# Kernel tuning notes

Hardware: AMD Instinct MI355X
Metric: run time of the kernel (lower is better)

The kernel has to match this reference:

```python
import jax, jax.numpy as jnp
import numpy as np

B, S, D = 2, 2048, 4096
NH, NKV, HD = 32, 8, 128
NREP = NH // NKV
ROPE_THETA = 10000.0


def setup_inputs() -> dict:
    key = jax.random.key(0)
    k1, k2, k3, k4, k5 = jax.random.split(key, 5)
    x = jax.random.normal(k1, (B, S, D), jnp.float32)
    wq = jax.random.normal(k2, (NH * HD, D), jnp.float32) * 0.02
    wk = jax.random.normal(k3, (NKV * HD, D), jnp.float32) * 0.02
    wv = jax.random.normal(k4, (NKV * HD, D), jnp.float32) * 0.02
    wo = jax.random.normal(k5, (D, NH * HD), jnp.float32) * 0.02
    inv_freq = 1.0 / (ROPE_THETA ** (np.arange(0, HD, 2, dtype=np.float64) / HD))
    ang = np.outer(np.arange(S, dtype=np.float64), inv_freq)  # [S, HD/2]
    return {
        'x': x, 'start_pos': 0,
        'freqs_cos': jnp.asarray(np.cos(ang), jnp.float32),
        'freqs_sin': jnp.asarray(np.sin(ang), jnp.float32),
        'wq': wq, 'wk': wk, 'wv': wv, 'wo': wo,
    }


def _apply_rope(x, cos, sin):
    # x: [B, S, H, HD]; cos/sin: [S, HD/2]. Matches torch view_as_complex on
    # interleaved (even, odd) feature pairs: (xr + i*xi) * (cos + i*sin).
    xr = x[..., 0::2]
    xi = x[..., 1::2]
    c = cos[None, :, None, :]
    s = sin[None, :, None, :]
    out_r = xr * c - xi * s
    out_i = xr * s + xi * c
    return jnp.stack([out_r, out_i], axis=-1).reshape(x.shape)


def reference(x, start_pos, freqs_cos, freqs_sin, wq, wk, wv, wo):
    b, s, _ = x.shape
    xq = (x @ wq.T).reshape(b, s, NH, HD)
    xk = (x @ wk.T).reshape(b, s, NKV, HD)
    xv = (x @ wv.T).reshape(b, s, NKV, HD)
    # Source applies RoPE to K and V (not Q) -- reproduced faithfully.
    xk = _apply_rope(xk, freqs_cos, freqs_sin)
    xv = _apply_rope(xv, freqs_cos, freqs_sin)
    # start_pos == 0 prefill: cache slice [:, :start_pos+s] == freshly written xk/xv.
    # repeat_kv: head h_out = h_kv * NREP + rep  ==  jnp.repeat along head axis.
    keys = jnp.repeat(xk, NREP, axis=2)    # [B, S, NH, HD]
    values = jnp.repeat(xv, NREP, axis=2)  # [B, S, NH, HD]
    scale = 1.0 / jnp.sqrt(jnp.asarray(HD, x.dtype))
    scores = jnp.einsum('bqhd,bkhd->bhqk', xq, keys) * scale  # [B, NH, S, S]
    probs = jax.nn.softmax(scores, axis=-1)  # NOTE: no causal mask in source
    out = jnp.einsum('bhqk,bkhd->bqhd', probs, values).reshape(b, s, NH * HD)
    return out @ wo.T
```

## Files before the change

### kernel.cpp

```cpp
#include <hip/hip_runtime.h>


typedef short bf16x8 __attribute__((ext_vector_type(8)));
typedef float f32x4 __attribute__((ext_vector_type(4)));

__device__ __forceinline__ void load16(const void* g, void* l) {
  __builtin_amdgcn_global_load_lds(
      (const __attribute__((address_space(1))) void*)g,
      (__attribute__((address_space(3))) void*)l, 16, 0, 0);
}

__device__ __forceinline__ f32x4 mfma16(bf16x8 a, bf16x8 b, f32x4 c) {
  return __builtin_amdgcn_mfma_f32_16x16x32_bf16(a, b, c, 0, 0, 0);
}

__device__ __forceinline__ unsigned short f2b(float f) {
  union { float f; unsigned int u; } v; v.f = f;
  unsigned int u = v.u;
  return (unsigned short)((u + 0x7fffu + ((u >> 16) & 1u)) >> 16);
}
__device__ __forceinline__ float b2f(unsigned short u) {
  union { unsigned int u; float f; } v; v.u = ((unsigned int)u) << 16;
  return v.f;
}

#define QSCALE (0.08838834764831845f * 1.4426950408889634f)

__global__ __launch_bounds__(256) void cvt_f32_bf16(
    const float* __restrict__ in, unsigned short* __restrict__ out, int n4) {
  int idx = blockIdx.x * 256 + threadIdx.x;
  int stride = gridDim.x * 256;
  for (int i = idx; i < n4; i += stride) {
    float4 v = reinterpret_cast<const float4*>(in)[i];
    ushort4 o;
    o.x = f2b(v.x); o.y = f2b(v.y); o.z = f2b(v.z); o.w = f2b(v.w);
    reinterpret_cast<ushort4*>(out)[i] = o;
  }
}

template <typename OutT, bool SCALEQ>
__global__ __launch_bounds__(512, 2) void gemm256(
    const unsigned short* __restrict__ A, const unsigned short* __restrict__ Bw,
    OutT* __restrict__ C, int M, int N, int K) {
  extern __shared__ char smem[];
  const int tid = threadIdx.x;
  const int lane = tid & 63;
  const int w = tid >> 6;
  const int lr = lane & 15, lg = lane >> 4;
  const int wr = w >> 2, wc = w & 3;

  const int nbn = N >> 8;
  const int bid = blockIdx.x, nwg = gridDim.x;
  const int swz = (bid & 7) * (nwg >> 3) + (bid >> 3);
  const int bm = swz / nbn, bn = swz % nbn;

  const unsigned short* Ag = A + (size_t)bm * 256 * K;
  const unsigned short* Bg = Bw + (size_t)bn * 256 * K;

  int srow[4], skhw[4], sdst[4];
#pragma unroll
  for (int j = 0; j < 4; ++j) {
    const int c = tid + j * 512;
    srow[j] = c >> 3;
    skhw[j] = ((c & 7) ^ ((c >> 3) & 7)) << 3;
    sdst[j] = ((tid & ~63) << 4) + j * 8192;
  }

  f32x4 acc[8][4];
#pragma unroll
  for (int m = 0; m < 8; ++m)
#pragma unroll
    for (int n = 0; n < 4; ++n) acc[m][n] = (f32x4){0.f, 0.f, 0.f, 0.f};

#define STAGEA4(tt)                                                           \
  {                                                                           \
    char* d = smem + (((tt)&1) * 65536);                                      \
    _Pragma("unroll") for (int j = 0; j < 4; ++j)                             \
        load16(Ag + (size_t)srow[j] * K + ((tt) << 6) + skhw[j], d + sdst[j]);\
  }
#define STAGEB4(tt)                                                           \
  {                                                                           \
    char* d = smem + (((tt)&1) * 65536) + 32768;                              \
    _Pragma("unroll") for (int j = 0; j < 4; ++j)                             \
        load16(Bg + (size_t)srow[j] * K + ((tt) << 6) + skhw[j], d + sdst[j]);\
  }

  STAGEB4(0);
  STAGEA4(0);

  const int NT = K >> 6;
  const int rx = (lr & 7) << 4;
  const int aRow0 = (wr * 128 + lr) * 128;
  const int bRow0 = (wc * 64 + lr) * 128;
  const int col0 = (lg * 16) ^ rx;
  const int col1 = (64 + lg * 16) ^ rx;

  bf16x8 aR[4][2], bR[4][2];

  for (int t = 0; t < NT; ++t) {
    const char* bufA = smem + (t & 1) * 65536;
    const char* bufB = bufA + 32768;
    const bool more = (t + 1) < NT;

    asm volatile("s_waitcnt vmcnt(0)" ::: "memory");
    __builtin_amdgcn_s_barrier();

#pragma unroll
    for (int mf = 0; mf < 4; ++mf) {
      aR[mf][0] = *(const bf16x8*)(bufA + aRow0 + mf * 2048 + col0);
      aR[mf][1] = *(const bf16x8*)(bufA + aRow0 + mf * 2048 + col1);
    }
#pragma unroll
    for (int nf = 0; nf < 2; ++nf) {
      bR[nf][0] = *(const bf16x8*)(bufB + bRow0 + nf * 2048 + col0);
      bR[nf][1] = *(const bf16x8*)(bufB + bRow0 + nf * 2048 + col1);
    }
    if (more) STAGEB4(t + 1);
    asm volatile("s_waitcnt lgkmcnt(8)" ::: "memory");
    __builtin_amdgcn_s_barrier();
    asm volatile("s_waitcnt lgkmcnt(0)" ::: "memory");
    __builtin_amdgcn_sched_barrier(0);
    __builtin_amdgcn_s_setprio(1);
#pragma unroll
    for (int mf = 0; mf < 4; ++mf)
#pragma unroll
      for (int nf = 0; nf < 2; ++nf) {
        acc[mf][nf] = mfma16(aR[mf][0], bR[nf][0], acc[mf][nf]);
        acc[mf][nf] = mfma16(aR[mf][1], bR[nf][1], acc[mf][nf]);
      }
    __builtin_amdgcn_s_setprio(0);
    __builtin_amdgcn_s_barrier();

#pragma unroll
    for (int nf = 2; nf < 4; ++nf) {
      bR[nf][0] = *(const bf16x8*)(bufB + bRow0 + nf * 2048 + col0);
      bR[nf][1] = *(const bf16x8*)(bufB + bRow0 + nf * 2048 + col1);
    }
    if (more) STAGEA4(t + 1);
    __builtin_amdgcn_s_barrier();
    asm volatile("s_waitcnt lgkmcnt(0)" ::: "memory");
    __builtin_amdgcn_sched_barrier(0);
    __builtin_amdgcn_s_setprio(1);
#pragma unroll
    for (int mf = 0; mf < 4; ++mf)
#pragma unroll
      for (int nf = 2; nf < 4; ++nf) {
        acc[mf][nf] = mfma16(aR[mf][0], bR[nf][0], acc[mf][nf]);
        acc[mf][nf] = mfma16(aR[mf][1], bR[nf][1], acc[mf][nf]);
      }
    __builtin_amdgcn_s_setprio(0);
    __builtin_amdgcn_s_barrier();

#pragma unroll
    for (int mf = 0; mf < 4; ++mf) {
      aR[mf][0] = *(const bf16x8*)(bufA + aRow0 + (4 + mf) * 2048 + col0);
      aR[mf][1] = *(const bf16x8*)(bufA + aRow0 + (4 + mf) * 2048 + col1);
    }
    __builtin_amdgcn_s_barrier();
    asm volatile("s_waitcnt lgkmcnt(0)" ::: "memory");
    __builtin_amdgcn_sched_barrier(0);
    __builtin_amdgcn_s_setprio(1);
#pragma unroll
    for (int mf = 0; mf < 4; ++mf)
#pragma unroll
      for (int nf = 0; nf < 2; ++nf) {
        acc[4 + mf][nf] = mfma16(aR[mf][0], bR[nf][0], acc[4 + mf][nf]);
        acc[4 + mf][nf] = mfma16(aR[mf][1], bR[nf][1], acc[4 + mf][nf]);
      }
    __builtin_amdgcn_s_setprio(0);
    __builtin_amdgcn_s_barrier();

    __builtin_amdgcn_s_setprio(1);
#pragma unroll
    for (int mf = 0; mf < 4; ++mf)
#pragma unroll
      for (int nf = 2; nf < 4; ++nf) {
        acc[4 + mf][nf] = mfma16(aR[mf][0], bR[nf][0], acc[4 + mf][nf]);
        acc[4 + mf][nf] = mfma16(aR[mf][1], bR[nf][1], acc[4 + mf][nf]);
      }
    __builtin_amdgcn_s_setprio(0);
  }
#undef STAGEA4
#undef STAGEB4

#pragma unroll
  for (int mf = 0; mf < 8; ++mf)
#pragma unroll
    for (int nf = 0; nf < 4; ++nf)
#pragma unroll
      for (int r = 0; r < 4; ++r) {
        int rowc = bm * 256 + wr * 128 + mf * 16 + lg * 4 + r;
        int colc = bn * 256 + wc * 64 + nf * 16 + lr;
        float v = acc[mf][nf][r];
        if constexpr (SCALEQ) v *= QSCALE;
        if constexpr (sizeof(OutT) == 2)
          C[(size_t)rowc * N + colc] = (OutT)f2b(v);
        else
          C[(size_t)rowc * N + colc] = v;
      }
}

template <typename OutT>
__global__ __launch_bounds__(256) void gemm_bt(
    const unsigned short* __restrict__ A, const unsigned short* __restrict__ Bw,
    OutT* __restrict__ C, int M, int N, int K) {
  alignas(16) __shared__ unsigned short As[4][128][8];
  alignas(16) __shared__ unsigned short Bs[4][128][8];
  const int t = threadIdx.x;
  const int lane = t & 63, w = t >> 6;
  const int lr = lane & 15, lg = lane >> 4;
  const int wr = w >> 1, wc = w & 1;

  const int nbn = N >> 7;
  const int nwg = gridDim.x;
  const int bid = blockIdx.x;
  const int swz = (bid & 7) * (nwg >> 3) + (bid >> 3);
  const int bm = swz / nbn, bn = swz % nbn;

  f32x4 acc[4][4];
#pragma unroll
  for (int m = 0; m < 4; ++m)
#pragma unroll
    for (int n = 0; n < 4; ++n) acc[m][n] = (f32x4){0.f, 0.f, 0.f, 0.f};

  const int c0 = t, c1 = 256 + t;
  const int kc0 = c0 >> 7, row0 = c0 & 127;
  const int kc1 = c1 >> 7, row1 = c1 & 127;
  const unsigned short* Ab = A + (size_t)(bm * 128) * K;
  const unsigned short* Bb = Bw + (size_t)(bn * 128) * K;
  char* AsB = (char*)&As[0][0][0];
  char* BsB = (char*)&Bs[0][0][0];
  const int ub0 = (t & 192) * 16;
  const int ub1 = (256 + (t & 192)) * 16;

  for (int k0 = 0; k0 < K; k0 += 32) {
    load16(Ab + (size_t)row0 * K + k0 + kc0 * 8, AsB + ub0);
    load16(Ab + (size_t)row1 * K + k0 + kc1 * 8, AsB + ub1);
    load16(Bb + (size_t)row0 * K + k0 + kc0 * 8, BsB + ub0);
    load16(Bb + (size_t)row1 * K + k0 + kc1 * 8, BsB + ub1);
    __syncthreads();
    bf16x8 af[4], bfr[4];
#pragma unroll
    for (int i = 0; i < 4; ++i)
      af[i] = *(const bf16x8*)&As[lg][wr * 64 + i * 16 + lr][0];
#pragma unroll
    for (int i = 0; i < 4; ++i)
      bfr[i] = *(const bf16x8*)&Bs[lg][wc * 64 + i * 16 + lr][0];
#pragma unroll
    for (int m = 0; m < 4; ++m)
#pragma unroll
      for (int n = 0; n < 4; ++n)
        acc[m][n] = mfma16(af[m], bfr[n], acc[m][n]);
    __syncthreads();
  }

#pragma unroll
  for (int m = 0; m < 4; ++m)
#pragma unroll
    for (int n = 0; n < 4; ++n)
#pragma unroll
      for (int r = 0; r < 4; ++r) {
        int rowc = bm * 128 + wr * 64 + m * 16 + lg * 4 + r;
        int colc = bn * 128 + wc * 64 + n * 16 + lr;
        float v = acc[m][n][r];
        if constexpr (sizeof(OutT) == 2)
          C[(size_t)rowc * N + colc] = (OutT)f2b(v);
        else
          C[(size_t)rowc * N + colc] = v;
      }
}

__global__ __launch_bounds__(256) void rope_kv(
    const unsigned short* __restrict__ XKV,
    const float* __restrict__ fc, const float* __restrict__ fs,
    unsigned short* __restrict__ Kr, unsigned short* __restrict__ Vt) {
  __shared__ unsigned short Vl[128][66];
  const int t = threadIdx.x;
  const int bid = blockIdx.x;
  const int stile = bid & 31, bkv = bid >> 5;
  const int b = bkv >> 3, kvh = bkv & 7;
  const int s0 = stile * 64;
  const int l = t & 63;
  const int jrow = t >> 6;

  for (int j = 0; j < 16; ++j) {
    int s = s0 + j * 4 + jrow;
    ushort2 v = *(const ushort2*)(XKV + (size_t)(b * 2048 + s) * 2048 + kvh * 128 + 2 * l);
    float c = fc[s * 64 + l], sn = fs[s * 64 + l];
    float xr = b2f(v.x), xi = b2f(v.y);
    ushort2 o;
    o.x = f2b(xr * c - xi * sn);
    o.y = f2b(xr * sn + xi * c);
    *(ushort2*)(Kr + ((size_t)bkv * 2048 + s) * 128 + 2 * l) = o;
  }
  for (int j = 0; j < 16; ++j) {
    int ss = j * 4 + jrow;
    int s = s0 + ss;
    ushort2 v = *(const ushort2*)(XKV + (size_t)(b * 2048 + s) * 2048 + 1024 + kvh * 128 + 2 * l);
    float c = fc[s * 64 + l], sn = fs[s * 64 + l];
    float xr = b2f(v.x), xi = b2f(v.y);
    Vl[2 * l][ss] = f2b(xr * c - xi * sn);
    Vl[2 * l + 1][ss] = f2b(xr * sn + xi * c);
  }
  __syncthreads();
  const int d = t >> 1, half = t & 1;
  unsigned short* vdst = Vt + ((size_t)bkv * 128 + d) * 2048 + s0 + half * 32;
#pragma unroll
  for (int e = 0; e < 32; e += 4) {
    ushort4 pk;
    pk.x = Vl[d][half * 32 + e];
    pk.y = Vl[d][half * 32 + e + 1];
    pk.z = Vl[d][half * 32 + e + 2];
    pk.w = Vl[d][half * 32 + e + 3];
    *(ushort4*)(vdst + e) = pk;
  }
}

__global__ __launch_bounds__(256, 2) void attn_fwd(
    const unsigned short* __restrict__ XQ, const unsigned short* __restrict__ Kr,
    const unsigned short* __restrict__ Vt, unsigned short* __restrict__ AO) {
  extern __shared__ char smem[];
  char* Ksm = smem;
  char* Vsm = smem + 32768;
  unsigned short* Ps = (unsigned short*)(smem + 65536);
  const int t = threadIdx.x;
  const int lane = t & 63, w = t >> 6;
  const int lr = lane & 15, lg = lane >> 4;

  const int bid = blockIdx.x;
  const int nwg = gridDim.x;
  const int swz = (bid & 7) * (nwg >> 3) + (bid >> 3);
  const int qt = swz & 15;
  const int bh = swz >> 4;
  const int b = bh >> 5, h = bh & 31;
  const int bkv = b * 8 + (h >> 2);

  bf16x8 qf[2][4];
#pragma unroll
  for (int q2 = 0; q2 < 2; ++q2) {
    const unsigned short* qp =
        XQ + ((size_t)(b * 2048 + qt * 128 + w * 32 + q2 * 16 + lr)) * 4096 +
        h * 128 + lg * 8;
#pragma unroll
    for (int dc = 0; dc < 4; ++dc) qf[q2][dc] = *(const bf16x8*)(qp + dc * 32);
  }

  f32x4 acc[2][8];
#pragma unroll
  for (int q2 = 0; q2 < 2; ++q2)
#pragma unroll
    for (int i = 0; i < 8; ++i) acc[q2][i] = (f32x4){0.f, 0.f, 0.f, 0.f};
  float l_[2][4] = {{0.f, 0.f, 0.f, 0.f}, {0.f, 0.f, 0.f, 0.f}};

  const unsigned short* Kbase = Kr + (size_t)bkv * 2048 * 128;
  const unsigned short* Vbase = Vt + (size_t)bkv * 128 * 2048;

  int kK[4], dC[4], vD[4], vKc[4], dstb[4];
#pragma unroll
  for (int j = 0; j < 4; ++j) {
    const int c = t + j * 256;
    kK[j] = c & 63;  dC[j] = c >> 6;
    vD[j] = c & 127; vKc[j] = c >> 7;
    dstb[j] = (c & ~63) * 16;
  }

#define STAGE_KV(bufi, kt)                                                    \
  {                                                                           \
    char* kd = Ksm + (bufi)*16384;                                            \
    char* vd = Vsm + (bufi)*16384;                                            \
    _Pragma("unroll") for (int j = 0; j < 4; ++j) {                           \
      load16(Kbase + (size_t)((kt)*64 + kK[j]) * 128 + dC[j] * 8, kd + dstb[j]); \
      load16(Vbase + (size_t)vD[j] * 2048 + (kt)*64 + vKc[j] * 8, vd + dstb[j]); \
    }                                                                         \
  }

  STAGE_KV(0, 0);
  asm volatile("s_waitcnt vmcnt(0)" ::: "memory");
  __builtin_amdgcn_s_barrier();

  unsigned short* Pw = Ps + w * 2048;
  const int pbase = (lr >> 3) * 256 + (lr & 7);

  for (int kt = 0; kt < 32; ++kt) {
    const int cur = kt & 1;
    if (kt < 31) STAGE_KV(cur ^ 1, kt + 1);

    const char* Kc = Ksm + cur * 16384;
    const char* Vc = Vsm + cur * 16384;

#pragma unroll
    for (int nf = 0; nf < 4; ++nf) {
      f32x4 s0 = (f32x4){0.f, 0.f, 0.f, 0.f};
      f32x4 s1 = (f32x4){0.f, 0.f, 0.f, 0.f};
#pragma unroll
      for (int dc = 0; dc < 4; ++dc) {
        bf16x8 kf =
            *(const bf16x8*)(Kc + ((dc * 4 + lg) * 64 + nf * 16 + lr) * 16);
        s0 = mfma16(qf[0][dc], kf, s0);
        s1 = mfma16(qf[1][dc], kf, s1);
      }
      const int pb = pbase + nf * 512;
#pragma unroll
      for (int r = 0; r < 4; ++r) {
        float p0 = __builtin_amdgcn_exp2f(s0[r]);
        float p1 = __builtin_amdgcn_exp2f(s1[r]);
        l_[0][r] += p0;
        l_[1][r] += p1;
        Pw[pb + (lg * 4 + r) * 8] = f2b(p0);
        Pw[pb + (16 + lg * 4 + r) * 8] = f2b(p1);
      }
    }

#pragma unroll
    for (int ks = 0; ks < 2; ++ks) {
      bf16x8 pf0 = *(const bf16x8*)(Pw + (ks * 4 + lg) * 256 + lr * 8);
      bf16x8 pf1 = *(const bf16x8*)(Pw + (ks * 4 + lg) * 256 + (16 + lr) * 8);
#pragma unroll
      for (int dt = 0; dt < 8; ++dt) {
        bf16x8 vf =
            *(const bf16x8*)(Vc + ((ks * 4 + lg) * 128 + dt * 16 + lr) * 16);
        acc[0][dt] = mfma16(pf0, vf, acc[0][dt]);
        acc[1][dt] = mfma16(pf1, vf, acc[1][dt]);
      }
    }

    asm volatile("s_waitcnt vmcnt(0)" ::: "memory");
    __builtin_amdgcn_s_barrier();
  }
#undef STAGE_KV

#pragma unroll
  for (int q2 = 0; q2 < 2; ++q2)
#pragma unroll
    for (int r = 0; r < 4; ++r) {
#pragma unroll
      for (int o = 1; o < 16; o <<= 1) l_[q2][r] += __shfl_xor(l_[q2][r], o);
    }

#pragma unroll
  for (int q2 = 0; q2 < 2; ++q2)
#pragma unroll
    for (int r = 0; r < 4; ++r) {
      float inv = 1.f / l_[q2][r];
      size_t rowb =
          ((size_t)(b * 2048 + qt * 128 + w * 32 + q2 * 16 + lg * 4 + r)) * 4096 +
          h * 128;
#pragma unroll
      for (int dt = 0; dt < 8; ++dt)
        AO[rowb + dt * 16 + lr] = f2b(acc[q2][dt][r] * inv);
    }
}

extern "C" void kernel_launch(void* const* d_in, const int* in_sizes, int n_in,
                              void* d_out, int out_size, void* d_ws, size_t ws_size,
                              hipStream_t stream) {
  const float* x  = (const float*)d_in[0];
  const float* fc = (const float*)d_in[2];
  const float* fs = (const float*)d_in[3];
  const float* wq = (const float*)d_in[4];
  const float* wk = (const float*)d_in[5];
  const float* wv = (const float*)d_in[6];
  const float* wo = (const float*)d_in[7];

  const size_t MB = 1024ull * 1024ull;
  char* ws = (char*)d_ws;
  unsigned short* Xb  = (unsigned short*)(ws);
  unsigned short* Wsc = (unsigned short*)(ws + 32 * MB);
  unsigned short* XKV = (unsigned short*)(ws + 64 * MB);
  unsigned short* Kr  = (unsigned short*)(ws);
  unsigned short* Vt  = (unsigned short*)(ws + 8 * MB);
  unsigned short* AO  = (unsigned short*)(ws + 80 * MB);
  unsigned short* XQ  = (unsigned short*)d_out;

  (void)hipFuncSetAttribute((const void*)gemm256<unsigned short, true>,
                            hipFuncAttributeMaxDynamicSharedMemorySize, 131072);
  (void)hipFuncSetAttribute((const void*)gemm256<float, false>,
                            hipFuncAttributeMaxDynamicSharedMemorySize, 131072);
  (void)hipFuncSetAttribute((const void*)attn_fwd,
                            hipFuncAttributeMaxDynamicSharedMemorySize, 81920);

  dim3 blk(256);
  dim3 blk512(512);
  cvt_f32_bf16<<<2048, blk, 0, stream>>>(x, Xb, (2 * 2048 * 4096) / 4);
  cvt_f32_bf16<<<2048, blk, 0, stream>>>(wq, Wsc, (4096 * 4096) / 4);
  gemm256<unsigned short, true><<<256, blk512, 131072, stream>>>(
      Xb, Wsc, XQ, 4096, 4096, 4096);
  cvt_f32_bf16<<<2048, blk, 0, stream>>>(wk, Wsc, (1024 * 4096) / 4);
  cvt_f32_bf16<<<2048, blk, 0, stream>>>(wv, Wsc + 1024 * 4096, (1024 * 4096) / 4);
  gemm_bt<unsigned short><<<512, blk, 0, stream>>>(Xb, Wsc, XKV, 4096, 2048, 4096);
  rope_kv<<<512, blk, 0, stream>>>(XKV, fc, fs, Kr, Vt);
  attn_fwd<<<1024, blk, 81920, stream>>>(XQ, Kr, Vt, AO);
  cvt_f32_bf16<<<2048, blk, 0, stream>>>(wo, Wsc, (4096 * 4096) / 4);
  gemm256<float, false><<<256, blk512, 131072, stream>>>(
      AO, Wsc, (float*)d_out, 4096, 4096, 4096);
}
```

Before: 597.6 us.

## Fuse Q, K and V projections into one gemm256 launch with per-column scaling

Concatenates the bf16 Wq, Wk and Wv weights into one buffer and computes Q, K and V with a single 256-tile GEMM of width 6144. This replaces the separate, simpler 128-tile gemm_bt used for K and V. The Q scale is applied only to the first 16 column blocks through a runtime threshold, and the rope and attention kernels now read from the interleaved 6144-stride output. It also swaps the hand-written bf16 rounding for the HIP __float2bfloat16 intrinsic in the attention P and output stores, which could change rounding slightly.

```diff
diff --git a/kernel.cpp b/kernel.cpp
--- a/kernel.cpp
+++ b/kernel.cpp
@@ -1,4 +1,5 @@
 #include <hip/hip_runtime.h>
+#include <hip/hip_bf16.h>
 
 
 typedef short bf16x8 __attribute__((ext_vector_type(8)));
@@ -22,6 +23,10 @@
 __device__ __forceinline__ float b2f(unsigned short u) {
   union { unsigned int u; float f; } v; v.u = ((unsigned int)u) << 16;
   return v.f;
+}
+__device__ __forceinline__ unsigned short f2b_fast(float f) {
+  __hip_bfloat16 h = __float2bfloat16(f);
+  return *reinterpret_cast<unsigned short*>(&h);
 }
 
 #define QSCALE (0.08838834764831845f * 1.4426950408889634f)
@@ -38,10 +43,10 @@
   }
 }
 
-template <typename OutT, bool SCALEQ>
+template <typename OutT>
 __global__ __launch_bounds__(512, 2) void gemm256(
     const unsigned short* __restrict__ A, const unsigned short* __restrict__ Bw,
-    OutT* __restrict__ C, int M, int N, int K) {
+    OutT* __restrict__ C, int M, int N, int K, int sbl) {
   extern __shared__ char smem[];
   const int tid = threadIdx.x;
   const int lane = tid & 63;
@@ -183,6 +188,7 @@
 #undef STAGEA4
 #undef STAGEB4
 
+  const float cscale = (bn < sbl) ? QSCALE : 1.0f;
 #pragma unroll
   for (int mf = 0; mf < 8; ++mf)
 #pragma unroll
@@ -191,8 +197,7 @@
       for (int r = 0; r < 4; ++r) {
         int rowc = bm * 256 + wr * 128 + mf * 16 + lg * 4 + r;
         int colc = bn * 256 + wc * 64 + nf * 16 + lr;
-        float v = acc[mf][nf][r];
-        if constexpr (SCALEQ) v *= QSCALE;
+        float v = acc[mf][nf][r] * cscale;
         if constexpr (sizeof(OutT) == 2)
           C[(size_t)rowc * N + colc] = (OutT)f2b(v);
         else
@@ -200,78 +205,8 @@
       }
 }
 
-template <typename OutT>
-__global__ __launch_bounds__(256) void gemm_bt(
-    const unsigned short* __restrict__ A, const unsigned short* __restrict__ Bw,
-    OutT* __restrict__ C, int M, int N, int K) {
-  alignas(16) __shared__ unsigned short As[4][128][8];
-  alignas(16) __shared__ unsigned short Bs[4][128][8];
-  const int t = threadIdx.x;
-  const int lane = t & 63, w = t >> 6;
-  const int lr = lane & 15, lg = lane >> 4;
-  const int wr = w >> 1, wc = w & 1;
-
-  const int nbn = N >> 7;
-  const int nwg = gridDim.x;
-  const int bid = blockIdx.x;
-  const int swz = (bid & 7) * (nwg >> 3) + (bid >> 3);
-  const int bm = swz / nbn, bn = swz % nbn;
-
-  f32x4 acc[4][4];
-#pragma unroll
-  for (int m = 0; m < 4; ++m)
-#pragma unroll
-    for (int n = 0; n < 4; ++n) acc[m][n] = (f32x4){0.f, 0.f, 0.f, 0.f};
-
-  const int c0 = t, c1 = 256 + t;
-  const int kc0 = c0 >> 7, row0 = c0 & 127;
-  const int kc1 = c1 >> 7, row1 = c1 & 127;
-  const unsigned short* Ab = A + (size_t)(bm * 128) * K;
-  const unsigned short* Bb = Bw + (size_t)(bn * 128) * K;
-  char* AsB = (char*)&As[0][0][0];
-  char* BsB = (char*)&Bs[0][0][0];
-  const int ub0 = (t & 192) * 16;
-  const int ub1 = (256 + (t & 192)) * 16;
-
-  for (int k0 = 0; k0 < K; k0 += 32) {
-    load16(Ab + (size_t)row0 * K + k0 + kc0 * 8, AsB + ub0);
-    load16(Ab + (size_t)row1 * K + k0 + kc1 * 8, AsB + ub1);
-    load16(Bb + (size_t)row0 * K + k0 + kc0 * 8, BsB + ub0);
-    load16(Bb + (size_t)row1 * K + k0 + kc1 * 8, BsB + ub1);
-    __syncthreads();
-    bf16x8 af[4], bfr[4];
-#pragma unroll
-    for (int i = 0; i < 4; ++i)
-      af[i] = *(const bf16x8*)&As[lg][wr * 64 + i * 16 + lr][0];
-#pragma unroll
-    for (int i = 0; i < 4; ++i)
-      bfr[i] = *(const bf16x8*)&Bs[lg][wc * 64 + i * 16 + lr][0];
-#pragma unroll
-    for (int m = 0; m < 4; ++m)
-#pragma unroll
-      for (int n = 0; n < 4; ++n)
-        acc[m][n] = mfma16(af[m], bfr[n], acc[m][n]);
-    __syncthreads();
-  }
-
-#pragma unroll
-  for (int m = 0; m < 4; ++m)
-#pragma unroll
-    for (int n = 0; n < 4; ++n)
-#pragma unroll
-      for (int r = 0; r < 4; ++r) {
-        int rowc = bm * 128 + wr * 64 + m * 16 + lg * 4 + r;
-        int colc = bn * 128 + wc * 64 + n * 16 + lr;
-        float v = acc[m][n][r];
-        if constexpr (sizeof(OutT) == 2)
-          C[(size_t)rowc * N + colc] = (OutT)f2b(v);
-        else
-          C[(size_t)rowc * N + colc] = v;
-      }
-}
-
 __global__ __launch_bounds__(256) void rope_kv(
-    const unsigned short* __restrict__ XKV,
+    const unsigned short* __restrict__ XQKV,
     const float* __restrict__ fc, const float* __restrict__ fs,
     unsigned short* __restrict__ Kr, unsigned short* __restrict__ Vt) {
   __shared__ unsigned short Vl[128][66];
@@ -285,7 +220,8 @@
 
   for (int j = 0; j < 16; ++j) {
     int s = s0 + j * 4 + jrow;
-    ushort2 v = *(const ushort2*)(XKV + (size_t)(b * 2048 + s) * 2048 + kvh * 128 + 2 * l);
+    ushort2 v = *(const ushort2*)(XQKV + (size_t)(b * 2048 + s) * 6144 + 4096 +
+                                  kvh * 128 + 2 * l);
     float c = fc[s * 64 + l], sn = fs[s * 64 + l];
     float xr = b2f(v.x), xi = b2f(v.y);
     ushort2 o;
@@ -296,7 +232,8 @@
   for (int j = 0; j < 16; ++j) {
     int ss = j * 4 + jrow;
     int s = s0 + ss;
-    ushort2 v = *(const ushort2*)(XKV + (size_t)(b * 2048 + s) * 2048 + 1024 + kvh * 128 + 2 * l);
+    ushort2 v = *(const ushort2*)(XQKV + (size_t)(b * 2048 + s) * 6144 + 5120 +
+                                  kvh * 128 + 2 * l);
     float c = fc[s * 64 + l], sn = fs[s * 64 + l];
     float xr = b2f(v.x), xi = b2f(v.y);
     Vl[2 * l][ss] = f2b(xr * c - xi * sn);
@@ -339,7 +276,7 @@
 #pragma unroll
   for (int q2 = 0; q2 < 2; ++q2) {
     const unsigned short* qp =
-        XQ + ((size_t)(b * 2048 + qt * 128 + w * 32 + q2 * 16 + lr)) * 4096 +
+        XQ + ((size_t)(b * 2048 + qt * 128 + w * 32 + q2 * 16 + lr)) * 6144 +
         h * 128 + lg * 8;
 #pragma unroll
     for (int dc = 0; dc < 4; ++dc) qf[q2][dc] = *(const bf16x8*)(qp + dc * 32);
@@ -406,8 +343,8 @@
         float p1 = __builtin_amdgcn_exp2f(s1[r]);
         l_[0][r] += p0;
         l_[1][r] += p1;
-        Pw[pb + (lg * 4 + r) * 8] = f2b(p0);
-        Pw[pb + (16 + lg * 4 + r) * 8] = f2b(p1);
+        Pw[pb + (lg * 4 + r) * 8] = f2b_fast(p0);
+        Pw[pb + (16 + lg * 4 + r) * 8] = f2b_fast(p1);
       }
     }
 
@@ -447,7 +384,7 @@
           h * 128;
 #pragma unroll
       for (int dt = 0; dt < 8; ++dt)
-        AO[rowb + dt * 16 + lr] = f2b(acc[q2][dt][r] * inv);
+        AO[rowb + dt * 16 + lr] = f2b_fast(acc[q2][dt][r] * inv);
     }
 }
 
@@ -464,17 +401,16 @@
 
   const size_t MB = 1024ull * 1024ull;
   char* ws = (char*)d_ws;
-  unsigned short* Xb  = (unsigned short*)(ws);
-  unsigned short* Wsc = (unsigned short*)(ws + 32 * MB);
-  unsigned short* XKV = (unsigned short*)(ws + 64 * MB);
-  unsigned short* Kr  = (unsigned short*)(ws);
-  unsigned short* Vt  = (unsigned short*)(ws + 8 * MB);
-  unsigned short* AO  = (unsigned short*)(ws + 80 * MB);
-  unsigned short* XQ  = (unsigned short*)d_out;
-
-  (void)hipFuncSetAttribute((const void*)gemm256<unsigned short, true>,
+  unsigned short* Xb   = (unsigned short*)(ws);
+  unsigned short* Wsc  = (unsigned short*)(ws + 32 * MB);
+  unsigned short* Kr   = (unsigned short*)(ws);
+  unsigned short* Vt   = (unsigned short*)(ws + 8 * MB);
+  unsigned short* AO   = (unsigned short*)(ws + 80 * MB);
+  unsigned short* XQKV = (unsigned short*)d_out;
+
+  (void)hipFuncSetAttribute((const void*)gemm256<unsigned short>,
                             hipFuncAttributeMaxDynamicSharedMemorySize, 131072);
-  (void)hipFuncSetAttribute((const void*)gemm256<float, false>,
+  (void)hipFuncSetAttribute((const void*)gemm256<float>,
                             hipFuncAttributeMaxDynamicSharedMemorySize, 131072);
   (void)hipFuncSetAttribute((const void*)attn_fwd,
                             hipFuncAttributeMaxDynamicSharedMemorySize, 81920);
@@ -483,14 +419,13 @@
   dim3 blk512(512);
   cvt_f32_bf16<<<2048, blk, 0, stream>>>(x, Xb, (2 * 2048 * 4096) / 4);
   cvt_f32_bf16<<<2048, blk, 0, stream>>>(wq, Wsc, (4096 * 4096) / 4);
-  gemm256<unsigned short, true><<<256, blk512, 131072, stream>>>(
-      Xb, Wsc, XQ, 4096, 4096, 4096);
-  cvt_f32_bf16<<<2048, blk, 0, stream>>>(wk, Wsc, (1024 * 4096) / 4);
-  cvt_f32_bf16<<<2048, blk, 0, stream>>>(wv, Wsc + 1024 * 4096, (1024 * 4096) / 4);
-  gemm_bt<unsigned short><<<512, blk, 0, stream>>>(Xb, Wsc, XKV, 4096, 2048, 4096);
-  rope_kv<<<512, blk, 0, stream>>>(XKV, fc, fs, Kr, Vt);
-  attn_fwd<<<1024, blk, 81920, stream>>>(XQ, Kr, Vt, AO);
+  cvt_f32_bf16<<<2048, blk, 0, stream>>>(wk, Wsc + 4096 * 4096, (1024 * 4096) / 4);
+  cvt_f32_bf16<<<2048, blk, 0, stream>>>(wv, Wsc + 5120 * 4096, (1024 * 4096) / 4);
+  gemm256<unsigned short><<<384, blk512, 131072, stream>>>(
+      Xb, Wsc, XQKV, 4096, 6144, 4096, 16);
+  rope_kv<<<512, blk, 0, stream>>>(XQKV, fc, fs, Kr, Vt);
+  attn_fwd<<<1024, blk, 81920, stream>>>(XQKV, Kr, Vt, AO);
   cvt_f32_bf16<<<2048, blk, 0, stream>>>(wo, Wsc, (4096 * 4096) / 4);
-  gemm256<float, false><<<256, blk512, 131072, stream>>>(
-      AO, Wsc, (float*)d_out, 4096, 4096, 4096);
-}
+  gemm256<float><<<256, blk512, 131072, stream>>>(
+      AO, Wsc, (float*)d_out, 4096, 4096, 4096, 0);
+}
```

Result: faster. 563.2 us (-5.8%).
